# Kernel tuning notes

Measured on AMD Instinct MI355X. Metric: run time of the kernel, lower is better.

## Reference

```python
import jax, jax.numpy as jnp
import numpy as np

B, T, V, E, U = 64, 512, 32000, 1024, 1024


def setup_inputs() -> dict:
    key = jax.random.key(0)
    k0, k1, k2, k3 = jax.random.split(key, 4)
    x = jax.random.randint(k0, (B, T), 0, V, dtype=jnp.int32)
    hidden = jnp.zeros((B, U), jnp.float32)
    emb = jax.random.normal(k1, (V, E), jnp.float32) * 0.02
    Wx = jax.random.normal(k2, (E, 3 * U), jnp.float32) / np.sqrt(E).astype(np.float32)
    Wh = jax.random.normal(k3, (U, 3 * U), jnp.float32) / np.sqrt(U).astype(np.float32)
    b_i = jnp.zeros((3 * U,), jnp.float32)  # input bias (reset_after=True has 2 biases)
    b_r = jnp.zeros((3 * U,), jnp.float32)  # recurrent bias
    return {"x": x, "hidden": hidden, "emb": emb, "Wx": Wx, "Wh": Wh, "b_i": b_i, "b_r": b_r}


def reference(x, hidden, emb, Wx, Wh, b_i, b_r):
    # Embedding with mask_zero=True: mask = (token != 0)
    mask = (x != 0)                                   # [B,T]
    e = jnp.take(emb, x, axis=0)                      # [B,T,E]
    # Precompute all input projections in one big GEMM (z|r|h gate order, Keras layout)
    xp = jnp.einsum('bte,eu->btu', e, Wx) + b_i       # [B,T,3U]
    xp_t = jnp.moveaxis(xp, 1, 0)                     # [T,B,3U] time-major for scan
    m_t = jnp.moveaxis(mask, 1, 0)[..., None]         # [T,B,1]

    def step(h, inp):
        xpt, m = inp
        hp = h @ Wh + b_r                             # [B,3U]
        xz, xr, xh = jnp.split(xpt, 3, axis=-1)
        hz, hr, hh = jnp.split(hp, 3, axis=-1)
        z = jax.nn.sigmoid(xz + hz)
        r = jax.nn.sigmoid(xr + hr)
        cand = jnp.tanh(xh + r * hh)                  # reset_after=True: r applied post-matmul
        h_new = z * h + (1.0 - z) * cand
        h_new = jnp.where(m, h_new, h)                # masked steps copy state through
        return h_new, h_new

    state, out_t = jax.lax.scan(step, hidden, (xp_t, m_t))
    output = jnp.moveaxis(out_t, 0, 1)                # [B,T,U]
    return output, state
```

## Files before the change

### kernel.cpp

```cpp
#include <hip/hip_runtime.h>
#include <stdint.h>


#define B_SZ   64
#define T_LEN  512
#define U_DIM  1024
#define E_DIM  1024
#define G3     3072
#define BU     (B_SZ * U_DIM)
#define XP_SCALE 131072.0f
#define XP_INV   (1.0f / 131072.0f)
#define H_SCALE  32768.0f
#define H_INV    (1.0f / 32768.0f)
#define LDT    40
#define NWG    256
#define GRPWG  64

typedef unsigned short ushort_t;
typedef __attribute__((ext_vector_type(8))) short bf16x8;
typedef __attribute__((ext_vector_type(4))) float f32x4;

__device__ __forceinline__ ushort_t f2bf(float f) {
  unsigned u = __builtin_bit_cast(unsigned, f);
  u += 0x7fffu + ((u >> 16) & 1u);
  return (ushort_t)(u >> 16);
}
__device__ __forceinline__ float bf2f(ushort_t h) {
  return __builtin_bit_cast(float, (unsigned)h << 16);
}

__device__ __forceinline__ bf16x8 ldg_cohere_b128(const void* p) {
  bf16x8 r;
  asm volatile("global_load_dwordx4 %0, %1, off sc0 sc1"
               : "=v"(r) : "v"(p) : "memory");
  return r;
}
__device__ __forceinline__ void stg_cohere_u16(short* p, unsigned v) {
  asm volatile("global_store_short %0, %1, off sc0 sc1"
               :: "v"(p), "v"(v) : "memory");
}
__device__ __forceinline__ unsigned ldg_cohere_u32(const unsigned* p) {
  unsigned r;
  asm volatile("global_load_dword %0, %1, off sc0 sc1\n\ts_waitcnt vmcnt(0)"
               : "=v"(r) : "v"(p) : "memory");
  return r;
}
__device__ __forceinline__ int ldg_sshort(const short* p) {
  int r;
  asm volatile("global_load_sshort %0, %1, off"
               : "=v"(r) : "v"(p) : "memory");
  return r;
}
__device__ __forceinline__ int ldg_s32(const int* p) {
  int r;
  asm volatile("global_load_dword %0, %1, off"
               : "=v"(r) : "v"(p) : "memory");
  return r;
}
__device__ __forceinline__ void stg_u32(float* p, float v) {
  asm volatile("global_store_dword %0, %1, off"
               :: "v"(p), "v"(v) : "memory");
}
#define WAITV(n) do { asm volatile("s_waitcnt vmcnt(" #n ")" ::: "memory"); \
                      __builtin_amdgcn_sched_barrier(0); } while (0)

__global__ __launch_bounds__(256) void gemm_xp(
    const float* __restrict__ emb,
    const float* __restrict__ Wx,
    const int* __restrict__ x,
    const float* __restrict__ b_i,
    short* __restrict__ xp)
{
  __shared__ ushort_t aH[128 * LDT];
  __shared__ ushort_t aL[128 * LDT];
  __shared__ ushort_t bH[128 * LDT];
  __shared__ ushort_t bL[128 * LDT];
  const int tid = threadIdx.x, lane = tid & 63, w = tid >> 6;
  const int bx = blockIdx.x;
  const int nIdx = bx % 24, mIdx = bx / 24;
  const int m0 = mIdx * 128, n0 = nIdx * 128;

  const int aRow0 = tid >> 2, aRow1 = (tid + 256) >> 2, aKoct = tid & 3;
  const size_t aBase0 = (size_t)x[m0 + aRow0] * E_DIM + (size_t)aKoct * 8;
  const size_t aBase1 = (size_t)x[m0 + aRow1] * E_DIM + (size_t)aKoct * 8;
  const int bN = tid & 127, bKoct0 = tid >> 7;

  const int wr = (w >> 1) * 64, wc = (w & 1) * 64;
  f32x4 acc[4][4];
#pragma unroll
  for (int i = 0; i < 4; i++)
#pragma unroll
    for (int j = 0; j < 4; j++) acc[i][j] = (f32x4){0.f, 0.f, 0.f, 0.f};

  for (int k0 = 0; k0 < E_DIM; k0 += 32) {
    __syncthreads();
#pragma unroll
    for (int pp = 0; pp < 2; ++pp) {
      const float* src = emb + (pp ? aBase1 : aBase0) + k0;
      int row = pp ? aRow1 : aRow0;
      float4 v0 = *(const float4*)(src);
      float4 v1 = *(const float4*)(src + 4);
      float vv[8] = {v0.x, v0.y, v0.z, v0.w, v1.x, v1.y, v1.z, v1.w};
      bf16x8 oh, ol;
#pragma unroll
      for (int j = 0; j < 8; ++j) {
        ushort_t hi = f2bf(vv[j]);
        oh[j] = (short)hi;
        ol[j] = (short)f2bf(vv[j] - bf2f(hi));
      }
      int off = row * LDT + aKoct * 8;
      *(bf16x8*)&aH[off] = oh;
      *(bf16x8*)&aL[off] = ol;
    }
#pragma unroll
    for (int kk = 0; kk < 2; ++kk) {
      int koct = bKoct0 + 2 * kk;
      float vv[8];
#pragma unroll
      for (int e = 0; e < 8; ++e)
        vv[e] = Wx[(size_t)(k0 + koct * 8 + e) * G3 + n0 + bN];
      bf16x8 oh, ol;
#pragma unroll
      for (int j = 0; j < 8; ++j) {
        ushort_t hi = f2bf(vv[j]);
        oh[j] = (short)hi;
        ol[j] = (short)f2bf(vv[j] - bf2f(hi));
      }
      int off = bN * LDT + koct * 8;
      *(bf16x8*)&bH[off] = oh;
      *(bf16x8*)&bL[off] = ol;
    }
    __syncthreads();
    bf16x8 afH[4], afL[4], bfH[4], bfL[4];
#pragma unroll
    for (int mi = 0; mi < 4; mi++) {
      int off = (wr + mi * 16 + (lane & 15)) * LDT + (lane >> 4) * 8;
      afH[mi] = *(const bf16x8*)&aH[off];
      afL[mi] = *(const bf16x8*)&aL[off];
    }
#pragma unroll
    for (int ni = 0; ni < 4; ni++) {
      int off = (wc + ni * 16 + (lane & 15)) * LDT + (lane >> 4) * 8;
      bfH[ni] = *(const bf16x8*)&bH[off];
      bfL[ni] = *(const bf16x8*)&bL[off];
    }
#pragma unroll
    for (int mi = 0; mi < 4; mi++)
#pragma unroll
      for (int ni = 0; ni < 4; ni++) {
        acc[mi][ni] = __builtin_amdgcn_mfma_f32_16x16x32_bf16(afH[mi], bfH[ni], acc[mi][ni], 0, 0, 0);
        acc[mi][ni] = __builtin_amdgcn_mfma_f32_16x16x32_bf16(afH[mi], bfL[ni], acc[mi][ni], 0, 0, 0);
        acc[mi][ni] = __builtin_amdgcn_mfma_f32_16x16x32_bf16(afL[mi], bfH[ni], acc[mi][ni], 0, 0, 0);
      }
  }
#pragma unroll
  for (int ni = 0; ni < 4; ni++) {
    int col = n0 + wc + ni * 16 + (lane & 15);
    float bias = b_i[col];
#pragma unroll
    for (int mi = 0; mi < 4; mi++) {
      int rbase = m0 + wr + mi * 16 + (lane >> 4) * 4;
#pragma unroll
      for (int i = 0; i < 4; i++) {
        int m = rbase + i;
        int b = m >> 9, t = m & 511;
        float v = acc[mi][ni][i] + bias;
        int q = __float2int_rn(v * XP_SCALE);
        q = q > 32767 ? 32767 : (q < -32768 ? -32768 : q);
        xp[(size_t)(t * 64 + b) * G3 + col] = (short)q;
      }
    }
  }
}

__global__ __launch_bounds__(256) void init_h(
    const float* __restrict__ hidden,
    short* __restrict__ h16,
    unsigned* __restrict__ cnt)
{
  const int i = blockIdx.x * 256 + threadIdx.x;
  if (blockIdx.x == 0 && threadIdx.x < 256) cnt[threadIdx.x] = 0u;
  if (i < BU) {
    int q = __float2int_rn(hidden[i] * H_SCALE);
    q = q > 32767 ? 32767 : (q < -32768 ? -32768 : q);
    h16[i] = (short)q;
  }
}

__global__ __launch_bounds__(512) void gru_scan(
    const float* __restrict__ hidden,
    const float* __restrict__ Wh,
    const float* __restrict__ b_r,
    const short* __restrict__ xp,
    const int* __restrict__ x,
    short* __restrict__ h16,
    unsigned* __restrict__ cnt,
    float* __restrict__ out)
{
  __shared__ float part[8][3][64][4];
  const int tid  = threadIdx.x;
  const int lane = tid & 63;
  const int w    = tid >> 6;
  const int bx   = (int)blockIdx.x;
  const int uj   = bx & 63, bi = bx >> 6;
  const int u0   = uj * 16, b0 = bi * 16;
  const int c16  = lane & 15;
  const int kg   = lane >> 4;
  unsigned* mycnt = cnt + bi * 64;

  bf16x8 BH[4][3], BL[4][3];
#pragma unroll
  for (int ks = 0; ks < 4; ++ks)
#pragma unroll
    for (int g = 0; g < 3; ++g) {
      bf16x8 bh, bl;
#pragma unroll
      for (int j = 0; j < 8; ++j) {
        int k = w * 128 + ks * 32 + kg * 8 + j;
        float v = Wh[(size_t)k * G3 + g * 1024 + u0 + c16];
        ushort_t hi = f2bf(v);
        bh[j] = (short)hi;
        bl[j] = (short)f2bf(v - bf2f(hi));
      }
      BH[ks][g] = bh;
      BL[ks][g] = bl;
    }

  const bool epi = (tid < 256);
  const int ebl = (tid >> 4) & 15, eul = tid & 15;
  const int eb = b0 + ebl, eu = u0 + eul;
  float brz = 0.f, brr = 0.f, brh = 0.f, hp = 0.f;
  if (epi) {
    brz = b_r[eu]; brr = b_r[1024 + eu]; brh = b_r[2048 + eu];
    hp  = hidden[(size_t)eb * U_DIM + eu];
  }

  asm volatile("s_waitcnt vmcnt(0) lgkmcnt(0)" ::: "memory");

  int xq0 = 0, xq1 = 0, xq2 = 0, xtok = 0;
  if (epi) {
    xq0 = ldg_sshort(xp + (size_t)eb * G3 + eu);
    xq1 = ldg_sshort(xp + (size_t)eb * G3 + 1024 + eu);
    xq2 = ldg_sshort(xp + (size_t)eb * G3 + 2048 + eu);
    xtok = ldg_s32(x + eb * T_LEN + 0);
  }

  unsigned target = 0;
  unsigned spins = 0;
  for (int t = 0; t < T_LEN; ++t) {
    const short* __restrict__ rP = h16 + (size_t)(t & 1) * BU;
    short* __restrict__ wP       = h16 + (size_t)((t + 1) & 1) * BU;

    const short* pP = rP + (size_t)(b0 + c16) * U_DIM + w * 128 + kg * 8;

    f32x4 acc[3];
#pragma unroll
    for (int g = 0; g < 3; ++g) acc[g] = (f32x4){0.f, 0.f, 0.f, 0.f};

    bf16x8 P0, P1, P2, P3;
    P0 = ldg_cohere_b128(pP + 0 * 32);
    P1 = ldg_cohere_b128(pP + 1 * 32);
    P2 = ldg_cohere_b128(pP + 2 * 32);
    P3 = ldg_cohere_b128(pP + 3 * 32);

#define UNPCK(P_, AH_, AL_) \
    { \
      _Pragma("unroll") \
      for (int j = 0; j < 8; ++j) { \
        float v = (float)(short)P_[j] * H_INV; \
        ushort_t hi = f2bf(v); \
        AH_[j] = (short)hi; \
        AL_[j] = (short)f2bf(v - bf2f(hi)); \
      } \
    }
#define COMP(AH_, AL_, ks_) \
    _Pragma("unroll") \
    for (int g = 0; g < 3; ++g) { \
      acc[g] = __builtin_amdgcn_mfma_f32_16x16x32_bf16(AH_, BH[ks_][g], acc[g], 0, 0, 0); \
      acc[g] = __builtin_amdgcn_mfma_f32_16x16x32_bf16(AH_, BL[ks_][g], acc[g], 0, 0, 0); \
      acc[g] = __builtin_amdgcn_mfma_f32_16x16x32_bf16(AL_, BH[ks_][g], acc[g], 0, 0, 0); \
    }
    bf16x8 AH, AL;
    WAITV(3);
    UNPCK(P0, AH, AL)
    COMP(AH, AL, 0)
    WAITV(2);
    UNPCK(P1, AH, AL)
    COMP(AH, AL, 1)
    WAITV(1);
    UNPCK(P2, AH, AL)
    COMP(AH, AL, 2)
    WAITV(0);
    UNPCK(P3, AH, AL)
    COMP(AH, AL, 3)
#undef UNPCK
#undef COMP

#pragma unroll
    for (int g = 0; g < 3; ++g)
      *(f32x4*)&part[w][g][lane][0] = acc[g];

    __syncthreads();

    if (epi) {
      const int pl = (ebl >> 2) * 16 + eul, pe = ebl & 3;
      float sz = 0.f, sr = 0.f, sh = 0.f;
#pragma unroll
      for (int s = 0; s < 8; ++s) {
        sz += part[s][0][pl][pe];
        sr += part[s][1][pl][pe];
        sh += part[s][2][pl][pe];
      }

      const float hz = sz + brz, hr = sr + brr, hhv = sh + brh;
      const float xz = (float)xq0 * XP_INV;
      const float xr = (float)xq1 * XP_INV;
      const float xh = (float)xq2 * XP_INV;
      const float z = 1.f / (1.f + __expf(-(xz + hz)));
      const float r = 1.f / (1.f + __expf(-(xr + hr)));
      const float ca = xh + r * hhv;
      const float cand = 1.f - 2.f / (__expf(2.f * ca) + 1.f);
      float hn = z * hp + (1.f - z) * cand;
      hn = (xtok != 0) ? hn : hp;
      hp = hn;

      stg_u32(&out[((size_t)eb * T_LEN + t) * U_DIM + eu], hn);
      int q = __float2int_rn(hn * H_SCALE);
      q = q > 32767 ? 32767 : (q < -32768 ? -32768 : q);
      stg_cohere_u16(wP + (size_t)eb * U_DIM + eu, (unsigned)q);

      const int tp = (t < T_LEN - 1) ? t + 1 : t;
      xq0 = ldg_sshort(xp + ((size_t)tp * B_SZ + eb) * G3 + eu);
      xq1 = ldg_sshort(xp + ((size_t)tp * B_SZ + eb) * G3 + 1024 + eu);
      xq2 = ldg_sshort(xp + ((size_t)tp * B_SZ + eb) * G3 + 2048 + eu);
      xtok = ldg_s32(x + eb * T_LEN + tp);
      WAITV(4);
    }

    target += GRPWG;
    __syncthreads();
    if (tid == 0)
      __hip_atomic_fetch_add(mycnt, 1u, __ATOMIC_RELAXED, __HIP_MEMORY_SCOPE_AGENT);
    if (w == 0) {
      while (spins < (1u << 22)) {
        if (ldg_cohere_u32(mycnt) >= target) break;
        __builtin_amdgcn_s_sleep(2);
        ++spins;
      }
    }
    __syncthreads();
    __builtin_amdgcn_sched_barrier(0);
  }

  if (epi)
    out[(size_t)B_SZ * T_LEN * U_DIM + (size_t)eb * U_DIM + eu] = hp;
}

extern "C" void kernel_launch(void* const* d_in, const int* in_sizes, int n_in,
                              void* d_out, int out_size, void* d_ws, size_t ws_size,
                              hipStream_t stream) {
  const int*   x      = (const int*)  d_in[0];
  const float* hidden = (const float*)d_in[1];
  const float* emb    = (const float*)d_in[2];
  const float* Wx     = (const float*)d_in[3];
  const float* Wh     = (const float*)d_in[4];
  const float* b_i    = (const float*)d_in[5];
  const float* b_r    = (const float*)d_in[6];
  float* out = (float*)d_out;

  const size_t XP_B = (size_t)T_LEN * B_SZ * G3 * 2;
  const size_t NEED = XP_B + 4 * (size_t)BU + 1024;
  if (ws_size < NEED) return;

  short*    xp  = (short*)d_ws;
  short*    h16 = (short*)((char*)d_ws + XP_B);
  unsigned* cnt = (unsigned*)(h16 + 2 * (size_t)BU);

  init_h<<<BU / 256, 256, 0, stream>>>(hidden, h16, cnt);
  gemm_xp<<<(32768 / 128) * (G3 / 128), 256, 0, stream>>>(emb, Wx, x, b_i, xp);
  gru_scan<<<NWG, 512, 0, stream>>>(hidden, Wh, b_r, xp, x, h16, cnt, out);
}
```

Baseline: 3.020 ms.

## Replace atomic counter barrier with per-workgroup step flags polled at step start

Each workgroup in a batch group now stores its step number to its own flag word instead of atomically incrementing a shared counter. Every wave polls all 64 flags of its group (8 per wave, 8 lanes each, combined with a ballot) at the start of the next step, so the trailing second __syncthreads and the wave-0-only spin are removed. The aim is to cut atomic contention and barrier latency on the per-timestep grid synchronisation. In exchange every wave now issues extra coherent loads while polling, and correctness depends on release ordering between the h16 stores and the flag store.

```diff
diff --git a/kernel.cpp b/kernel.cpp
--- a/kernel.cpp
+++ b/kernel.cpp
@@ -14,7 +14,6 @@
 #define H_INV    (1.0f / 32768.0f)
 #define LDT    40
 #define NWG    256
-#define GRPWG  64
 
 typedef unsigned short ushort_t;
 typedef __attribute__((ext_vector_type(8))) short bf16x8;
@@ -37,6 +36,10 @@
 }
 __device__ __forceinline__ void stg_cohere_u16(short* p, unsigned v) {
   asm volatile("global_store_short %0, %1, off sc0 sc1"
+               :: "v"(p), "v"(v) : "memory");
+}
+__device__ __forceinline__ void stg_cohere_u32(unsigned* p, unsigned v) {
+  asm volatile("global_store_dword %0, %1, off sc0 sc1"
                :: "v"(p), "v"(v) : "memory");
 }
 __device__ __forceinline__ unsigned ldg_cohere_u32(const unsigned* p) {
@@ -176,10 +179,10 @@
 __global__ __launch_bounds__(256) void init_h(
     const float* __restrict__ hidden,
     short* __restrict__ h16,
-    unsigned* __restrict__ cnt)
+    unsigned* __restrict__ flags)
 {
   const int i = blockIdx.x * 256 + threadIdx.x;
-  if (blockIdx.x == 0 && threadIdx.x < 256) cnt[threadIdx.x] = 0u;
+  if (blockIdx.x == 0) flags[threadIdx.x] = 0u;
   if (i < BU) {
     int q = __float2int_rn(hidden[i] * H_SCALE);
     q = q > 32767 ? 32767 : (q < -32768 ? -32768 : q);
@@ -194,7 +197,7 @@
     const short* __restrict__ xp,
     const int* __restrict__ x,
     short* __restrict__ h16,
-    unsigned* __restrict__ cnt,
+    unsigned* __restrict__ flags,
     float* __restrict__ out)
 {
   __shared__ float part[8][3][64][4];
@@ -206,7 +209,8 @@
   const int u0   = uj * 16, b0 = bi * 16;
   const int c16  = lane & 15;
   const int kg   = lane >> 4;
-  unsigned* mycnt = cnt + bi * 64;
+  unsigned* gflags = flags + bi * 64;
+  const unsigned* pollp = gflags + 8 * w + (lane & 7);
 
   bf16x8 BH[4][3], BL[4][3];
 #pragma unroll
@@ -245,11 +249,20 @@
     xtok = ldg_s32(x + eb * T_LEN + 0);
   }
 
-  unsigned target = 0;
   unsigned spins = 0;
   for (int t = 0; t < T_LEN; ++t) {
     const short* __restrict__ rP = h16 + (size_t)(t & 1) * BU;
     short* __restrict__ wP       = h16 + (size_t)((t + 1) & 1) * BU;
+
+    if (t > 0) {
+      const unsigned tgt = (unsigned)t;
+      while (spins < (1u << 22)) {
+        unsigned f = ldg_cohere_u32(pollp);
+        if (__ballot(f >= tgt) == ~0ull) break;
+        __builtin_amdgcn_s_sleep(1);
+        ++spins;
+      }
+    }
 
     const short* pP = rP + (size_t)(b0 + c16) * U_DIM + w * 128 + kg * 8;
 
@@ -337,18 +350,9 @@
       WAITV(4);
     }
 
-    target += GRPWG;
     __syncthreads();
     if (tid == 0)
-      __hip_atomic_fetch_add(mycnt, 1u, __ATOMIC_RELAXED, __HIP_MEMORY_SCOPE_AGENT);
-    if (w == 0) {
-      while (spins < (1u << 22)) {
-        if (ldg_cohere_u32(mycnt) >= target) break;
-        __builtin_amdgcn_s_sleep(2);
-        ++spins;
-      }
-    }
-    __syncthreads();
+      stg_cohere_u32(gflags + uj, (unsigned)(t + 1));
     __builtin_amdgcn_sched_barrier(0);
   }
 
@@ -372,11 +376,11 @@
   const size_t NEED = XP_B + 4 * (size_t)BU + 1024;
   if (ws_size < NEED) return;
 
-  short*    xp  = (short*)d_ws;
-  short*    h16 = (short*)((char*)d_ws + XP_B);
-  unsigned* cnt = (unsigned*)(h16 + 2 * (size_t)BU);
-
-  init_h<<<BU / 256, 256, 0, stream>>>(hidden, h16, cnt);
+  short*    xp    = (short*)d_ws;
+  short*    h16   = (short*)((char*)d_ws + XP_B);
+  unsigned* flags = (unsigned*)(h16 + 2 * (size_t)BU);
+
+  init_h<<<BU / 256, 256, 0, stream>>>(hidden, h16, flags);
   gemm_xp<<<(32768 / 128) * (G3 / 128), 256, 0, stream>>>(emb, Wx, x, b_i, xp);
-  gru_scan<<<NWG, 512, 0, stream>>>(hidden, Wh, b_r, xp, x, h16, cnt, out);
-}
+  gru_scan<<<NWG, 512, 0, stream>>>(hidden, Wh, b_r, xp, x, h16, flags, out);
+}
```

After: 3.768 ms. 24.8% more time.
